# Kernel optimization log

Measured on AMD Instinct MI355X. Metric: run time of the kernel, lower is better.

The kernel has to match this reference:

```python
import jax, jax.numpy as jnp
import numpy as np

B, T, D = 64, 4096, 256


def setup_inputs() -> dict:
    key = jax.random.key(0)
    k0, k1, k2, k3 = jax.random.split(key, 4)
    q = jax.random.normal(k0, (B, D), dtype=jnp.float32)
    k = jax.random.normal(k1, (B, T, D), dtype=jnp.float32)
    m = jax.random.uniform(k2, (B, T), dtype=jnp.float32)
    # learned params: torch.rand init for weights, zeros for bias
    W = jax.random.uniform(k3, (D, D), dtype=jnp.float32)
    bias = jnp.zeros((1,), dtype=jnp.float32)
    return {"q": q, "k": k, "m": m, "W": W, "bias": bias}


def reference(q, k, m, W, bias):
    # mids = W @ q   (original repeats W over batch; a single einsum suffices)
    mids = jnp.einsum('de,be->bd', W, q)            # [B, D]
    # scores_bt = tanh(k_bt . mids_b + bias)
    scores = jnp.tanh(jnp.einsum('btd,bd->bt', k, mids) + bias)  # [B, T]
    # masked, max-stabilized softmax over time
    scores = scores - jnp.max(scores, axis=1, keepdims=True)
    e = jnp.exp(scores) * m
    attn = e / jnp.sum(e, axis=1, keepdims=True)
    return attn
```

## Files before the change

### kernel.cpp

```cpp
#include <hip/hip_runtime.h>
#include <math.h>


#define BB 64
#define TT 4096
#define DD 256
#define TBLKS 32
#define RPB (TT / TBLKS)
#define GB 8
#define CHUNK (TT / GB)

template<int CTRL>
__device__ __forceinline__ float dpp_add(float x) {
    int xi = __builtin_bit_cast(int, x);
    int yi = __builtin_amdgcn_update_dpp(0, xi, CTRL, 0xF, 0xF, true);
    return x + __builtin_bit_cast(float, yi);
}
__device__ __forceinline__ float row16_sum(float p) {
    p = dpp_add<0xB1>(p);
    p = dpp_add<0x4E>(p);
    p = dpp_add<0x141>(p);
    p = dpp_add<0x140>(p);
    return p;
}

__device__ __forceinline__ float fast_tanh(float x) {
    float e = __expf(2.0f * x);
    return 1.0f - 2.0f * __builtin_amdgcn_rcpf(1.0f + e);
}

__global__ __launch_bounds__(256) void mids_kernel(const float* __restrict__ q,
                                                   const float* __restrict__ W,
                                                   float* __restrict__ mids) {
    const int b    = blockIdx.x;
    const int seg  = blockIdx.y;
    const int lane = threadIdx.x & 63;
    const int wave = threadIdx.x >> 6;
    const int grp  = lane >> 4;
    const int l16  = lane & 15;

    const float* qb = q + (size_t)b * DD + l16 * 4;
    const float4 qf0 = *(const float4*)(qb + 0);
    const float4 qf1 = *(const float4*)(qb + 64);
    const float4 qf2 = *(const float4*)(qb + 128);
    const float4 qf3 = *(const float4*)(qb + 192);

    const int d = seg * 16 + wave * 4 + grp;
    const float* wr = W + (size_t)d * DD + l16 * 4;
    const float4 w0 = *(const float4*)(wr + 0);
    const float4 w1 = *(const float4*)(wr + 64);
    const float4 w2 = *(const float4*)(wr + 128);
    const float4 w3 = *(const float4*)(wr + 192);
    float p = w0.x*qf0.x + w0.y*qf0.y + w0.z*qf0.z + w0.w*qf0.w;
    p += w1.x*qf1.x + w1.y*qf1.y + w1.z*qf1.z + w1.w*qf1.w;
    p += w2.x*qf2.x + w2.y*qf2.y + w2.z*qf2.z + w2.w*qf2.w;
    p += w3.x*qf3.x + w3.y*qf3.y + w3.z*qf3.z + w3.w*qf3.w;
    p = row16_sum(p);
    if (l16 == 0) mids[b * DD + d] = p;
}

__global__ __launch_bounds__(256) void fused_kernel(const float* __restrict__ k,
                                                    const float* __restrict__ mids,
                                                    const float* __restrict__ m,
                                                    const float* __restrict__ bias,
                                                    float* __restrict__ out,
                                                    float* __restrict__ blocksum) {
    const int b    = blockIdx.x;
    const int tb   = blockIdx.y;
    const int lane = threadIdx.x & 63;
    const int wave = threadIdx.x >> 6;
    const int grp  = lane >> 4;
    const int l16  = lane & 15;
    const float bv = bias[0];

    const float* mb = mids + (size_t)b * DD + l16 * 4;
    const float4 mf0 = *(const float4*)(mb + 0);
    const float4 mf1 = *(const float4*)(mb + 64);
    const float4 mf2 = *(const float4*)(mb + 128);
    const float4 mf3 = *(const float4*)(mb + 192);

    const int t0 = tb * RPB + wave * 32;
    const float* kbase = k + ((size_t)b * TT + t0) * DD + l16 * 4;
    const float* mrow  = m + (size_t)b * TT + t0;
    float* orow        = out + (size_t)b * TT + t0;

    float4 c0, c1, c2, c3, n0, n1, n2, n3;
    {
        const float* kr = kbase + (size_t)grp * DD;
        c0 = *(const float4*)(kr + 0);
        c1 = *(const float4*)(kr + 64);
        c2 = *(const float4*)(kr + 128);
        c3 = *(const float4*)(kr + 192);
    }
    float esum = 0.0f;
    #pragma unroll
    for (int g = 0; g < 8; ++g) {
        if (g < 7) {
            const float* kr = kbase + (size_t)((g + 1) * 4 + grp) * DD;
            n0 = *(const float4*)(kr + 0);
            n1 = *(const float4*)(kr + 64);
            n2 = *(const float4*)(kr + 128);
            n3 = *(const float4*)(kr + 192);
        }
        float p = c0.x*mf0.x + c0.y*mf0.y + c0.z*mf0.z + c0.w*mf0.w;
        p += c1.x*mf1.x + c1.y*mf1.y + c1.z*mf1.z + c1.w*mf1.w;
        p += c2.x*mf2.x + c2.y*mf2.y + c2.z*mf2.z + c2.w*mf2.w;
        p += c3.x*mf3.x + c3.y*mf3.y + c3.z*mf3.z + c3.w*mf3.w;
        p = row16_sum(p);
        const float s = fast_tanh(p + bv);
        if (l16 == 0) {
            const int trow = g * 4 + grp;
            const float e = __expf(s) * mrow[trow];
            orow[trow] = e;
            esum += e;
        }
        c0 = n0; c1 = n1; c2 = n2; c3 = n3;
    }
    esum += __shfl_xor(esum, 16, 64);
    esum += __shfl_xor(esum, 32, 64);
    __shared__ float wsum[4];
    if (lane == 0) wsum[wave] = esum;
    __syncthreads();
    if (threadIdx.x == 0)
        blocksum[b * TBLKS + tb] = (wsum[0] + wsum[1]) + (wsum[2] + wsum[3]);
}

__global__ __launch_bounds__(256) void norm_kernel(const float* __restrict__ blocksum,
                                                   float* __restrict__ out) {
    const int b   = blockIdx.x;
    const int g   = blockIdx.y;
    const int tid = threadIdx.x;
    float s = 0.0f;
    #pragma unroll
    for (int i = 0; i < TBLKS; ++i) s += blocksum[b * TBLKS + i];
    const float inv = 1.0f / s;
    const int idx = b * TT + g * CHUNK + tid * 2;
    float2 v = *(const float2*)(out + idx);
    v.x *= inv; v.y *= inv;
    *(float2*)(out + idx) = v;
}

extern "C" void kernel_launch(void* const* d_in, const int* in_sizes, int n_in,
                              void* d_out, int out_size, void* d_ws, size_t ws_size,
                              hipStream_t stream) {
    const float* q    = (const float*)d_in[0];
    const float* k    = (const float*)d_in[1];
    const float* m    = (const float*)d_in[2];
    const float* W    = (const float*)d_in[3];
    const float* bias = (const float*)d_in[4];
    float* out = (float*)d_out;

    float* ws       = (float*)d_ws;
    float* mids     = ws;
    float* blocksum = mids + BB * DD;

    mids_kernel<<<dim3(BB, 16), 256, 0, stream>>>(q, W, mids);
    fused_kernel<<<dim3(BB, TBLKS), 256, 0, stream>>>(k, mids, m, bias, out, blocksum);
    norm_kernel<<<dim3(BB, GB), 256, 0, stream>>>(blocksum, out);
}
```

Baseline: 395.5 us.

## Stream k rows through double-buffered LDS via async global_load_lds; split mask-sum into separate kernel

The fused score kernel now copies k rows straight into a double-buffered LDS tile with async global-to-LDS loads, prefetching the next 16-row chunk while the current one is dotted with mids. Each thread then reads its row from LDS. The mask multiply and block sum move out of this kernel into a new sum kernel plus a finish kernel that reapplies the mask during normalisation. The aim is more bytes in flight and less register pressure in the bandwidth-bound k stream, at the cost of an extra launch, two barriers per chunk, and rereading m and out.

```diff
diff --git a/kernel.cpp b/kernel.cpp
--- a/kernel.cpp
+++ b/kernel.cpp
@@ -6,7 +6,9 @@
 #define TT 4096
 #define DD 256
 #define TBLKS 32
-#define RPB (TT / TBLKS)
+#define RPB 128
+#define CROWS 16
+#define NCH (RPB / CROWS)
 #define GB 8
 #define CHUNK (TT / GB)
 
@@ -27,6 +29,13 @@
 __device__ __forceinline__ float fast_tanh(float x) {
     float e = __expf(2.0f * x);
     return 1.0f - 2.0f * __builtin_amdgcn_rcpf(1.0f + e);
+}
+
+__device__ __forceinline__ void async_row1k(const float* g, float* lds) {
+    __builtin_amdgcn_global_load_lds(
+        (const __attribute__((address_space(1))) void*)g,
+        (__attribute__((address_space(3))) void*)lds,
+        16, 0, 0);
 }
 
 __global__ __launch_bounds__(256) void mids_kernel(const float* __restrict__ q,
@@ -59,19 +68,19 @@
     if (l16 == 0) mids[b * DD + d] = p;
 }
 
-__global__ __launch_bounds__(256) void fused_kernel(const float* __restrict__ k,
-                                                    const float* __restrict__ mids,
-                                                    const float* __restrict__ m,
-                                                    const float* __restrict__ bias,
-                                                    float* __restrict__ out,
-                                                    float* __restrict__ blocksum) {
-    const int b    = blockIdx.x;
-    const int tb   = blockIdx.y;
-    const int lane = threadIdx.x & 63;
-    const int wave = threadIdx.x >> 6;
-    const int grp  = lane >> 4;
-    const int l16  = lane & 15;
-    const float bv = bias[0];
+__global__ __launch_bounds__(256) void stream_kernel(const float* __restrict__ k,
+                                                     const float* __restrict__ mids,
+                                                     const float* __restrict__ bias,
+                                                     float* __restrict__ out) {
+    __shared__ float buf[2][CROWS * DD];
+    const int b     = blockIdx.x;
+    const int tb    = blockIdx.y;
+    const int tid   = threadIdx.x;
+    const int lane  = tid & 63;
+    const int wave  = tid >> 6;
+    const int l16   = lane & 15;
+    const int grp16 = tid >> 4;
+    const float bv  = bias[0];
 
     const float* mb = mids + (size_t)b * DD + l16 * 4;
     const float4 mf0 = *(const float4*)(mb + 0);
@@ -79,64 +88,78 @@
     const float4 mf2 = *(const float4*)(mb + 128);
     const float4 mf3 = *(const float4*)(mb + 192);
 
-    const int t0 = tb * RPB + wave * 32;
-    const float* kbase = k + ((size_t)b * TT + t0) * DD + l16 * 4;
-    const float* mrow  = m + (size_t)b * TT + t0;
-    float* orow        = out + (size_t)b * TT + t0;
+    const int t0 = tb * RPB;
+    const float* kb = k + ((size_t)b * TT + t0) * DD;
+    float* orow = out + (size_t)b * TT + t0;
 
-    float4 c0, c1, c2, c3, n0, n1, n2, n3;
     {
-        const float* kr = kbase + (size_t)grp * DD;
-        c0 = *(const float4*)(kr + 0);
-        c1 = *(const float4*)(kr + 64);
-        c2 = *(const float4*)(kr + 128);
-        c3 = *(const float4*)(kr + 192);
+        const float* src = kb + (size_t)(wave * 4) * DD + lane * 4;
+        float* dst = &buf[0][(wave * 4) * DD];
+        #pragma unroll
+        for (int j = 0; j < 4; ++j) async_row1k(src + j * DD, dst + j * DD);
     }
-    float esum = 0.0f;
-    #pragma unroll
-    for (int g = 0; g < 8; ++g) {
-        if (g < 7) {
-            const float* kr = kbase + (size_t)((g + 1) * 4 + grp) * DD;
-            n0 = *(const float4*)(kr + 0);
-            n1 = *(const float4*)(kr + 64);
-            n2 = *(const float4*)(kr + 128);
-            n3 = *(const float4*)(kr + 192);
+
+    for (int c = 0; c < NCH; ++c) {
+        if (c + 1 < NCH) {
+            const float* src = kb + (size_t)((c + 1) * CROWS + wave * 4) * DD + lane * 4;
+            float* dst = &buf[(c + 1) & 1][(wave * 4) * DD];
+            #pragma unroll
+            for (int j = 0; j < 4; ++j) async_row1k(src + j * DD, dst + j * DD);
         }
-        float p = c0.x*mf0.x + c0.y*mf0.y + c0.z*mf0.z + c0.w*mf0.w;
-        p += c1.x*mf1.x + c1.y*mf1.y + c1.z*mf1.z + c1.w*mf1.w;
-        p += c2.x*mf2.x + c2.y*mf2.y + c2.z*mf2.z + c2.w*mf2.w;
-        p += c3.x*mf3.x + c3.y*mf3.y + c3.z*mf3.z + c3.w*mf3.w;
+        __syncthreads();
+
+        const float* row = &buf[c & 1][grp16 * DD + l16 * 4];
+        const float4 r0 = *(const float4*)(row + 0);
+        const float4 r1 = *(const float4*)(row + 64);
+        const float4 r2 = *(const float4*)(row + 128);
+        const float4 r3 = *(const float4*)(row + 192);
+        float p = r0.x*mf0.x + r0.y*mf0.y + r0.z*mf0.z + r0.w*mf0.w;
+        p += r1.x*mf1.x + r1.y*mf1.y + r1.z*mf1.z + r1.w*mf1.w;
+        p += r2.x*mf2.x + r2.y*mf2.y + r2.z*mf2.z + r2.w*mf2.w;
+        p += r3.x*mf3.x + r3.y*mf3.y + r3.z*mf3.z + r3.w*mf3.w;
         p = row16_sum(p);
-        const float s = fast_tanh(p + bv);
-        if (l16 == 0) {
-            const int trow = g * 4 + grp;
-            const float e = __expf(s) * mrow[trow];
-            orow[trow] = e;
-            esum += e;
-        }
-        c0 = n0; c1 = n1; c2 = n2; c3 = n3;
+        const float e = __expf(fast_tanh(p + bv));
+        if (l16 == 0) orow[c * CROWS + grp16] = e;
+
+        __syncthreads();
     }
-    esum += __shfl_xor(esum, 16, 64);
-    esum += __shfl_xor(esum, 32, 64);
-    __shared__ float wsum[4];
-    if (lane == 0) wsum[wave] = esum;
-    __syncthreads();
-    if (threadIdx.x == 0)
-        blocksum[b * TBLKS + tb] = (wsum[0] + wsum[1]) + (wsum[2] + wsum[3]);
 }
 
-__global__ __launch_bounds__(256) void norm_kernel(const float* __restrict__ blocksum,
-                                                   float* __restrict__ out) {
+__global__ __launch_bounds__(256) void sum_kernel(const float* __restrict__ out,
+                                                  const float* __restrict__ m,
+                                                  float* __restrict__ bsum) {
+    const int b    = blockIdx.x;
+    const int g    = blockIdx.y;
+    const int tid  = threadIdx.x;
+    const int lane = tid & 63;
+    const int wave = tid >> 6;
+    __shared__ float wsum[4];
+
+    const int idx = b * TT + g * CHUNK + tid * 2;
+    const float2 ov = *(const float2*)(out + idx);
+    const float2 mv = *(const float2*)(m + idx);
+    float local = ov.x * mv.x + ov.y * mv.y;
+    #pragma unroll
+    for (int off = 32; off; off >>= 1) local += __shfl_xor(local, off, 64);
+    if (lane == 0) wsum[wave] = local;
+    __syncthreads();
+    if (tid == 0) bsum[b * GB + g] = (wsum[0] + wsum[1]) + (wsum[2] + wsum[3]);
+}
+
+__global__ __launch_bounds__(256) void finish_kernel(const float* __restrict__ m,
+                                                     const float* __restrict__ bsum,
+                                                     float* __restrict__ out) {
     const int b   = blockIdx.x;
     const int g   = blockIdx.y;
     const int tid = threadIdx.x;
     float s = 0.0f;
     #pragma unroll
-    for (int i = 0; i < TBLKS; ++i) s += blocksum[b * TBLKS + i];
+    for (int i = 0; i < GB; ++i) s += bsum[b * GB + i];
     const float inv = 1.0f / s;
     const int idx = b * TT + g * CHUNK + tid * 2;
     float2 v = *(const float2*)(out + idx);
-    v.x *= inv; v.y *= inv;
+    const float2 mv = *(const float2*)(m + idx);
+    v.x *= mv.x * inv; v.y *= mv.y * inv;
     *(float2*)(out + idx) = v;
 }
 
@@ -150,11 +173,12 @@
     const float* bias = (const float*)d_in[4];
     float* out = (float*)d_out;
 
-    float* ws       = (float*)d_ws;
-    float* mids     = ws;
-    float* blocksum = mids + BB * DD;
+    float* ws   = (float*)d_ws;
+    float* mids = ws;
+    float* bsum = mids + BB * DD;
 
     mids_kernel<<<dim3(BB, 16), 256, 0, stream>>>(q, W, mids);
-    fused_kernel<<<dim3(BB, TBLKS), 256, 0, stream>>>(k, mids, m, bias, out, blocksum);
-    norm_kernel<<<dim3(BB, GB), 256, 0, stream>>>(blocksum, out);
+    stream_kernel<<<dim3(BB, TBLKS), 256, 0, stream>>>(k, mids, bias, out);
+    sum_kernel<<<dim3(BB, GB), 256, 0, stream>>>(out, m, bsum);
+    finish_kernel<<<dim3(BB, GB), 256, 0, stream>>>(m, bsum, out);
 }
```

Result: faster. 371.9 us (-6.0%).
